# Kernel optimization log

Measured on AMD Instinct MI355X. Metric: run time of the kernel, lower is better.

The kernel has to match this reference:

```python
import jax, jax.numpy as jnp
import numpy as np

B, L, D, H, HD, K, MAXLEN = 4, 2048, 1024, 16, 64, 32, 2048


def setup_inputs() -> dict:
    key = jax.random.key(0)
    ks = jax.random.split(key, 8)
    s = 0.02  # init scale (stand-in for lecun-normal magnitude)
    return {
        "inputs_q": jax.random.normal(ks[0], (B, L, D), jnp.float32),
        "inputs_kv": jax.random.normal(ks[1], (B, L, D), jnp.float32),
        "Wv": jax.random.normal(ks[2], (D, H, HD), jnp.float32) * s,   # value DenseGeneral kernel
        "bv": jnp.zeros((H, HD), jnp.float32),                          # value bias
        "r1": jax.random.normal(ks[3], (H, MAXLEN, K), jnp.float32) * s,  # param 'random1'
        "r2": jax.random.normal(ks[4], (H, K, MAXLEN), jnp.float32) * s,  # param 'random2'
        "Wo": jax.random.normal(ks[5], (H, HD, D), jnp.float32) * s,   # output DenseGeneral kernel
        "bo": jnp.zeros((D,), jnp.float32),                             # output bias
    }


def reference(inputs_q, inputs_kv, Wv, bv, r1, r2, Wo, bo):
    # SynthesizerAttention with ignore_dot_product=True, mode='factorized_random',
    # no masks, deterministic (no dropout).
    qlen = inputs_q.shape[-2]
    kvlen = inputs_kv.shape[-2]
    # value projection: [B, Lkv, H, HD]; key=value, query=inputs_q (unused for scores)
    v = jnp.einsum('bnd,dhk->bnhk', inputs_kv, Wv) + bv
    # factorized random synthetic scores: [H, Lq, Lkv]
    syn = jnp.einsum('hlk,hkn->hln', r1[:, :qlen, :], r2[:, :, :kvlen])
    # softmax over the key/value axis (norm_dims in synthetic_attention).
    # Scores are batch-independent, so softmax once per head (broadcast over B).
    attn = jax.nn.softmax(syn, axis=-1)
    # weighted sum over values: [B, Lq, H, HD]
    y = jnp.einsum('hln,bnhk->blhk', attn, v)
    # output projection over (H, HD): [B, Lq, D]
    return jnp.einsum('blhk,hkd->bld', y, Wo) + bo
```

## Files before the change

kernel.cpp:

```cpp
#include <hip/hip_runtime.h>
#include <hip/hip_bf16.h>

#define LL 2048

typedef __bf16 bf16x8 __attribute__((ext_vector_type(8)));
typedef __bf16 bf16x4 __attribute__((ext_vector_type(4)));
typedef float f32x4 __attribute__((ext_vector_type(4)));

__device__ inline void gl_lds16(const __bf16* g, __bf16* l) {
    __builtin_amdgcn_global_load_lds((const __attribute__((address_space(1))) void*)g,
                                     (__attribute__((address_space(3))) void*)l, 16, 0, 0);
}

__global__ __launch_bounds__(256) void prep(const float* __restrict__ inputs_kv,
                                            const float* __restrict__ r1,
                                            const float* __restrict__ Wv,
                                            const float* __restrict__ Wo,
                                            const float* __restrict__ r2,
                                            __bf16* __restrict__ A1,
                                            __bf16* __restrict__ r1b,
                                            __bf16* __restrict__ Wvt,
                                            __bf16* __restrict__ Wot,
                                            __bf16* __restrict__ r2t) {
    __shared__ float Ls[32][65];
    int bid = blockIdx.x;
    const int tid = threadIdx.x;
    if (bid < 4608) {
        const float* in = (bid < 4096) ? inputs_kv : r1;
        __bf16* out = (bid < 4096) ? A1 : r1b;
        const int t = ((bid < 4096) ? bid : bid - 4096) * 256 + tid;
        const float4* in4 = (const float4*)in;
        float4 f0 = in4[t * 2], f1 = in4[t * 2 + 1];
        bf16x8 o;
        o[0] = (__bf16)f0.x; o[1] = (__bf16)f0.y; o[2] = (__bf16)f0.z; o[3] = (__bf16)f0.w;
        o[4] = (__bf16)f1.x; o[5] = (__bf16)f1.y; o[6] = (__bf16)f1.z; o[7] = (__bf16)f1.w;
        *(bf16x8*)&out[(size_t)t * 8] = o;
        return;
    }
    bid -= 4608;
    const float* in;
    __bf16* out;
    int R, C, r0, c0;
    if (bid < 512) {
        in = Wv; out = Wvt; R = 1024; C = 1024;
        c0 = (bid & 15) * 64; r0 = (bid >> 4) * 32;
    } else if (bid < 1024) {
        bid -= 512;
        in = Wo; out = Wot; R = 1024; C = 1024;
        c0 = (bid & 15) * 64; r0 = (bid >> 4) * 32;
    } else {
        bid -= 1024;
        const int bz = bid >> 5;
        in = r2 + (size_t)bz * 65536; out = r2t + (size_t)bz * 65536;
        R = 32; C = 2048;
        c0 = (bid & 31) * 64; r0 = 0;
    }
#pragma unroll
    for (int p = 0; p < 2; ++p) {
        int f = tid + 256 * p;
        int row = f >> 4, c4 = (f & 15) << 2;
        float4 v = *(const float4*)&in[(size_t)(r0 + row) * C + c0 + c4];
        Ls[row][c4 + 0] = v.x; Ls[row][c4 + 1] = v.y;
        Ls[row][c4 + 2] = v.z; Ls[row][c4 + 3] = v.w;
    }
    __syncthreads();
    const int orow = tid >> 2, rc = (tid & 3) << 3;
    bf16x8 o;
#pragma unroll
    for (int j = 0; j < 8; ++j) o[j] = (__bf16)Ls[rc + j][orow];
    *(bf16x8*)&out[(size_t)(c0 + orow) * R + r0 + rc] = o;
}

template <int MODE>
__global__ __launch_bounds__(256) void gemm_bt(const __bf16* __restrict__ A,
                                               const __bf16* __restrict__ Bt,
                                               const float* __restrict__ bias,
                                               void* __restrict__ Cout,
                                               int M, int N, int K) {
    __shared__ alignas(16) __bf16 As[2][128 * 32];
    const int tid = threadIdx.x;
    const int lane = tid & 63;
    const int wid = __builtin_amdgcn_readfirstlane(tid >> 6);
    const int f = blockIdx.y * 8 + blockIdx.x;
    const int g = (f & 7) * 64 + (f >> 3);
    const int row0 = (g >> 3) * 128, col0 = (g & 7) * 128;
    const int l15 = lane & 15, quad = lane >> 4;
    const int wr = wid & 1, wc = wid >> 1;
    const int s0 = wid * 2, s1 = s0 + 1;

    const __bf16* ga0 = A + (size_t)(row0 + s0 * 16 + (lane >> 2)) * K + ((lane & 3) << 3);
    const __bf16* ga1 = ga0 + (size_t)16 * K;
    const __bf16* gB = Bt + (size_t)(col0 + wc * 64 + l15) * K + quad * 8;

    f32x4 acc[4][4];
#pragma unroll
    for (int i = 0; i < 4; ++i)
#pragma unroll
        for (int j = 0; j < 4; ++j) acc[i][j] = (f32x4){0.f, 0.f, 0.f, 0.f};

    const int nt = K >> 5;
    gl_lds16(ga0, As[0] + s0 * 512);
    gl_lds16(ga1, As[0] + s1 * 512);
    bf16x8 bcur[4], bnxt[4];
#pragma unroll
    for (int j = 0; j < 4; ++j)
        bcur[j] = *(const bf16x8*)(gB + (size_t)j * 16 * K);

    for (int t = 0; t < nt; ++t) {
        __syncthreads();
        if (t + 1 < nt) {
            const int k0 = (t + 1) << 5;
            const int nb = (t + 1) & 1;
            gl_lds16(ga0 + k0, As[nb] + s0 * 512);
            gl_lds16(ga1 + k0, As[nb] + s1 * 512);
#pragma unroll
            for (int j = 0; j < 4; ++j)
                bnxt[j] = *(const bf16x8*)(gB + (size_t)j * 16 * K + k0);
        }
        const __bf16* as = As[t & 1];
        bf16x8 af[4];
#pragma unroll
        for (int i = 0; i < 4; ++i)
            af[i] = *(const bf16x8*)&as[(wr * 64 + i * 16 + l15) * 32 + quad * 8];
#pragma unroll
        for (int i = 0; i < 4; ++i)
#pragma unroll
            for (int j = 0; j < 4; ++j)
                acc[i][j] = __builtin_amdgcn_mfma_f32_16x16x32_bf16(af[i], bcur[j], acc[i][j], 0, 0, 0);
        if (t + 1 < nt) {
#pragma unroll
            for (int j = 0; j < 4; ++j) bcur[j] = bnxt[j];
        }
    }

#pragma unroll
    for (int i = 0; i < 4; ++i) {
        const int rg = row0 + wr * 64 + i * 16 + quad * 4;
#pragma unroll
        for (int j = 0; j < 4; ++j) {
            const int cg = col0 + wc * 64 + j * 16 + l15;
            const float bb = bias[cg];
            if (MODE == 0) {
                const int b = rg >> 11, n = rg & 2047;
                const int h = cg >> 6, hd = cg & 63;
                const int nc = n >> 6, ks = (n >> 5) & 1, qj = (n >> 3) & 3, j0 = n & 7;
                const int jt = hd >> 4, fl = hd & 15;
                __bf16* V3 = (__bf16*)Cout;
                bf16x4 v;
#pragma unroll
                for (int r = 0; r < 4; ++r) v[r] = (__bf16)(acc[i][j][r] + bb);
                *(bf16x4*)&V3[(size_t)(((h * 32 + nc) * 4 + b) * 4096) +
                              (jt * 2 + ks) * 512 + fl * 32 + qj * 8 + j0] = v;
            } else {
                float* Cf = (float*)Cout;
#pragma unroll
                for (int r = 0; r < 4; ++r)
                    Cf[(size_t)(rg + r) * N + cg] = acc[i][j][r] + bb;
            }
        }
    }
}

__global__ __launch_bounds__(512) void attn_pv_v7(const __bf16* __restrict__ r1b,
                                                  const __bf16* __restrict__ r2t,
                                                  const __bf16* __restrict__ V3,
                                                  __bf16* __restrict__ yb) {
    __shared__ alignas(16) __bf16 Ps[2 * 2 * 4 * 1024];
    const int tid = threadIdx.x;
    const int lane = tid & 63;
    const int w = __builtin_amdgcn_readfirstlane(tid >> 6);
    const int b = w & 3, lh = w >> 2;
    const int l15 = lane & 15, quad = lane >> 4;
    const int id = blockIdx.x;
    const int h = id & 15;
    const int l0 = (id >> 4) << 7;

    bf16x8 bf1[4];
#pragma unroll
    for (int i = 0; i < 4; ++i)
        bf1[i] = *(const bf16x8*)&r1b[(size_t)(h * 2048 + l0 + lh * 64 + i * 16 + l15) * 32 + quad * 8];

    const __bf16* r2p = r2t + (size_t)(h * 2048 + b * 16 + l15) * 32 + quad * 8;
    const __bf16* vp = V3 + (size_t)((h * 32) * 4 + b) * 4096 + l15 * 32 + quad * 8;

    bf16x8 r2f = *(const bf16x8*)r2p;
    bf16x8 vpf[4][2];
#pragma unroll
    for (int jt = 0; jt < 4; ++jt)
#pragma unroll
        for (int ks = 0; ks < 2; ++ks)
            vpf[jt][ks] = *(const bf16x8*)(vp + (jt * 2 + ks) * 512);

    bf16x8 ones;
#pragma unroll
    for (int e = 0; e < 8; ++e) ones[e] = (__bf16)1.0f;

    f32x4 acc[4][4];
    f32x4 den[4];
#pragma unroll
    for (int i = 0; i < 4; ++i) {
        den[i] = (f32x4){0.f, 0.f, 0.f, 0.f};
#pragma unroll
        for (int j = 0; j < 4; ++j) acc[i][j] = (f32x4){0.f, 0.f, 0.f, 0.f};
    }
    const f32x4 zero4 = {0.f, 0.f, 0.f, 0.f};

    const int kw = b >> 1;
    const int jg = (b & 1) * 2 + (quad >> 1);
    const int q4 = (quad & 1) * 4;
    const int swz = (l15 >> 1) & 3;

    f32x4 s[4];
#pragma unroll
    for (int i = 0; i < 4; ++i)
        s[i] = __builtin_amdgcn_mfma_f32_16x16x32_bf16(r2f, bf1[i], zero4, 0, 0, 0);
    r2f = *(const bf16x8*)(r2p + 2048);
    {
        __bf16* ps = &Ps[lh * 4096];
#pragma unroll
        for (int i = 0; i < 4; ++i) {
            bf16x4 p4;
#pragma unroll
            for (int r = 0; r < 4; ++r) p4[r] = (__bf16)__expf(s[i][r]);
            *(bf16x4*)&ps[i * 1024 + kw * 512 + l15 * 32 + ((jg ^ swz) << 3) + q4] = p4;
        }
    }

    for (int c = 0; c < 32; ++c) {
        asm volatile("s_waitcnt lgkmcnt(0)" ::: "memory");
        __builtin_amdgcn_s_barrier();
        const __bf16* ps_r = &Ps[((c & 1) * 2 + lh) * 4096];
        bf16x8 pa[4][2];
#pragma unroll
        for (int i = 0; i < 4; ++i)
#pragma unroll
            for (int ks = 0; ks < 2; ++ks)
                pa[i][ks] = *(const bf16x8*)&ps_r[i * 1024 + ks * 512 + l15 * 32 + ((quad ^ swz) << 3)];
#pragma unroll
        for (int i = 0; i < 4; ++i)
            s[i] = __builtin_amdgcn_mfma_f32_16x16x32_bf16(r2f, bf1[i], zero4, 0, 0, 0);
        const int i2 = (c < 30) ? (c + 2) : 31;
        r2f = *(const bf16x8*)(r2p + (size_t)i2 * 2048);
#pragma unroll
        for (int ks = 0; ks < 2; ++ks) {
#pragma unroll
            for (int i = 0; i < 4; ++i) {
#pragma unroll
                for (int jt = 0; jt < 4; ++jt)
                    acc[i][jt] = __builtin_amdgcn_mfma_f32_16x16x32_bf16(pa[i][ks], vpf[jt][ks],
                                                                         acc[i][jt], 0, 0, 0);
                den[i] = __builtin_amdgcn_mfma_f32_16x16x32_bf16(pa[i][ks], ones, den[i], 0, 0, 0);
            }
        }
        __bf16* ps_w = &Ps[(((c + 1) & 1) * 2 + lh) * 4096];
#pragma unroll
        for (int i = 0; i < 4; ++i) {
            bf16x4 p4;
#pragma unroll
            for (int r = 0; r < 4; ++r) p4[r] = (__bf16)__expf(s[i][r]);
            *(bf16x4*)&ps_w[i * 1024 + kw * 512 + l15 * 32 + ((jg ^ swz) << 3) + q4] = p4;
        }
        const int cv = (c < 31) ? 1 : 0;
        vp += cv * 16384;
#pragma unroll
        for (int jt = 0; jt < 4; ++jt)
#pragma unroll
            for (int ks = 0; ks < 2; ++ks)
                vpf[jt][ks] = *(const bf16x8*)(vp + (jt * 2 + ks) * 512);
    }

#pragma unroll
    for (int i = 0; i < 4; ++i) {
#pragma unroll
        for (int r = 0; r < 4; ++r) {
            const float iv = 1.0f / den[i][r];
            const int l = l0 + lh * 64 + i * 16 + quad * 4 + r;
            const size_t rowbase = ((size_t)b * LL + l) * 1024 + h * 64;
#pragma unroll
            for (int jt = 0; jt < 4; ++jt)
                yb[rowbase + jt * 16 + l15] = (__bf16)(acc[i][jt][r] * iv);
        }
    }
}

extern "C" void kernel_launch(void* const* d_in, const int* in_sizes, int n_in,
                              void* d_out, int out_size, void* d_ws, size_t ws_size,
                              hipStream_t stream) {
    const float* inputs_kv = (const float*)d_in[1];
    const float* Wv = (const float*)d_in[2];
    const float* bv = (const float*)d_in[3];
    const float* r1 = (const float*)d_in[4];
    const float* r2 = (const float*)d_in[5];
    const float* Wo = (const float*)d_in[6];
    const float* bo = (const float*)d_in[7];
    float* out = (float*)d_out;

    char* ws = (char*)d_ws;
    const size_t MB = 1024 * 1024;
    __bf16* A1  = (__bf16*)(ws);
    __bf16* Wvt = (__bf16*)(ws + 16 * MB);
    __bf16* Wot = (__bf16*)(ws + 18 * MB);
    __bf16* r1b = (__bf16*)(ws + 20 * MB);
    __bf16* r2t = (__bf16*)(ws + 22 * MB);
    __bf16* V3  = (__bf16*)(ws + 24 * MB);
    __bf16* yb  = (__bf16*)(ws + 40 * MB);

    prep<<<6144, 256, 0, stream>>>(inputs_kv, r1, Wv, Wo, r2, A1, r1b, Wvt, Wot, r2t);
    gemm_bt<0><<<dim3(8, 64), 256, 0, stream>>>(A1, Wvt, bv, V3, 8192, 1024, 1024);
    attn_pv_v7<<<256, 512, 0, stream>>>(r1b, r2t, V3, yb);
    gemm_bt<1><<<dim3(8, 64), 256, 0, stream>>>(yb, Wot, bo, out, 8192, 1024, 1024);
}
```

Before: 233.8 us.

## Stage B tiles through LDS with triple-buffered async loads in gemm_bt

The B operand in the projection GEMMs is now loaded into LDS through direct global-to-LDS copies instead of per-wave register loads, and both A and B use a three-stage ring buffer with prefetch distance two. Explicit vmcnt waits plus a raw barrier replace the single syncthreads, so loads for future tiles stay in flight during the MFMAs. This is meant to hide global load latency and remove the duplicated B fetches across waves. In exchange it uses more LDS, which can lower occupancy, and it relies on hand-counted vmcnt values being correct.

```diff
diff --git a/kernel.cpp b/kernel.cpp
--- a/kernel.cpp
+++ b/kernel.cpp
@@ -77,7 +77,8 @@
                                                const float* __restrict__ bias,
                                                void* __restrict__ Cout,
                                                int M, int N, int K) {
-    __shared__ alignas(16) __bf16 As[2][128 * 32];
+    __shared__ alignas(16) __bf16 As[3][128 * 32];
+    __shared__ alignas(16) __bf16 Bs[3][128 * 32];
     const int tid = threadIdx.x;
     const int lane = tid & 63;
     const int wid = __builtin_amdgcn_readfirstlane(tid >> 6);
@@ -90,7 +91,8 @@
 
     const __bf16* ga0 = A + (size_t)(row0 + s0 * 16 + (lane >> 2)) * K + ((lane & 3) << 3);
     const __bf16* ga1 = ga0 + (size_t)16 * K;
-    const __bf16* gB = Bt + (size_t)(col0 + wc * 64 + l15) * K + quad * 8;
+    const __bf16* gb0 = Bt + (size_t)(col0 + s0 * 16 + (lane >> 2)) * K + ((lane & 3) << 3);
+    const __bf16* gb1 = gb0 + (size_t)16 * K;
 
     f32x4 acc[4][4];
 #pragma unroll
@@ -99,38 +101,49 @@
         for (int j = 0; j < 4; ++j) acc[i][j] = (f32x4){0.f, 0.f, 0.f, 0.f};
 
     const int nt = K >> 5;
+
     gl_lds16(ga0, As[0] + s0 * 512);
     gl_lds16(ga1, As[0] + s1 * 512);
-    bf16x8 bcur[4], bnxt[4];
-#pragma unroll
-    for (int j = 0; j < 4; ++j)
-        bcur[j] = *(const bf16x8*)(gB + (size_t)j * 16 * K);
-
+    gl_lds16(gb0, Bs[0] + s0 * 512);
+    gl_lds16(gb1, Bs[0] + s1 * 512);
+    if (nt > 1) {
+        gl_lds16(ga0 + 32, As[1] + s0 * 512);
+        gl_lds16(ga1 + 32, As[1] + s1 * 512);
+        gl_lds16(gb0 + 32, Bs[1] + s0 * 512);
+        gl_lds16(gb1 + 32, Bs[1] + s1 * 512);
+    }
+
+    int cur = 0;
     for (int t = 0; t < nt; ++t) {
-        __syncthreads();
         if (t + 1 < nt) {
-            const int k0 = (t + 1) << 5;
-            const int nb = (t + 1) & 1;
+            asm volatile("s_waitcnt vmcnt(4)" ::: "memory");
+        } else {
+            asm volatile("s_waitcnt vmcnt(0)" ::: "memory");
+        }
+        __builtin_amdgcn_s_barrier();
+        if (t + 2 < nt) {
+            int nb = cur + 2; if (nb >= 3) nb -= 3;
+            const int k0 = (t + 2) << 5;
             gl_lds16(ga0 + k0, As[nb] + s0 * 512);
             gl_lds16(ga1 + k0, As[nb] + s1 * 512);
-#pragma unroll
-            for (int j = 0; j < 4; ++j)
-                bnxt[j] = *(const bf16x8*)(gB + (size_t)j * 16 * K + k0);
-        }
-        const __bf16* as = As[t & 1];
-        bf16x8 af[4];
+            gl_lds16(gb0 + k0, Bs[nb] + s0 * 512);
+            gl_lds16(gb1 + k0, Bs[nb] + s1 * 512);
+        }
+        const __bf16* as = As[cur];
+        const __bf16* bs = Bs[cur];
+        bf16x8 af[4], bfv[4];
 #pragma unroll
         for (int i = 0; i < 4; ++i)
             af[i] = *(const bf16x8*)&as[(wr * 64 + i * 16 + l15) * 32 + quad * 8];
 #pragma unroll
+        for (int j = 0; j < 4; ++j)
+            bfv[j] = *(const bf16x8*)&bs[(wc * 64 + j * 16 + l15) * 32 + quad * 8];
+#pragma unroll
         for (int i = 0; i < 4; ++i)
 #pragma unroll
             for (int j = 0; j < 4; ++j)
-                acc[i][j] = __builtin_amdgcn_mfma_f32_16x16x32_bf16(af[i], bcur[j], acc[i][j], 0, 0, 0);
-        if (t + 1 < nt) {
-#pragma unroll
-            for (int j = 0; j < 4; ++j) bcur[j] = bnxt[j];
-        }
+                acc[i][j] = __builtin_amdgcn_mfma_f32_16x16x32_bf16(af[i], bfv[j], acc[i][j], 0, 0, 0);
+        cur = (cur + 1 == 3) ? 0 : cur + 1;
     }
 
 #pragma unroll
```

New measurement: 211.2 us. 9.7% less time.

## Stage both GEMM operands through swizzled LDS with BK=64 double buffering

Applied to the files above, without the earlier changes.

The gemm_bt kernel now stages both A and B tiles into LDS with direct global-to-LDS loads, using a K-step of 64 instead of 32. An XOR swizzle on 16-byte chunks is meant to avoid LDS bank conflicts. Previously B fragments were loaded straight from global memory into registers, with each wave fetching them separately. The aim is to halve the number of barriers per K and to get B reuse and coalescing through LDS. The cost is four times the LDS footprint (64KB total), which may lower occupancy.

```diff
diff --git a/kernel.cpp b/kernel.cpp
--- a/kernel.cpp
+++ b/kernel.cpp
@@ -77,7 +77,8 @@
                                                const float* __restrict__ bias,
                                                void* __restrict__ Cout,
                                                int M, int N, int K) {
-    __shared__ alignas(16) __bf16 As[2][128 * 32];
+    __shared__ alignas(16) __bf16 As[2][128 * 64];
+    __shared__ alignas(16) __bf16 Bs[2][128 * 64];
     const int tid = threadIdx.x;
     const int lane = tid & 63;
     const int wid = __builtin_amdgcn_readfirstlane(tid >> 6);
@@ -86,11 +87,12 @@
     const int row0 = (g >> 3) * 128, col0 = (g & 7) * 128;
     const int l15 = lane & 15, quad = lane >> 4;
     const int wr = wid & 1, wc = wid >> 1;
-    const int s0 = wid * 2, s1 = s0 + 1;
-
-    const __bf16* ga0 = A + (size_t)(row0 + s0 * 16 + (lane >> 2)) * K + ((lane & 3) << 3);
-    const __bf16* ga1 = ga0 + (size_t)16 * K;
-    const __bf16* gB = Bt + (size_t)(col0 + wc * 64 + l15) * K + quad * 8;
+
+    const int srow = wid * 32 + (lane >> 3);
+    const int skoff = (((lane & 7) ^ (lane >> 3)) << 3);
+    const __bf16* gaS = A + (size_t)(row0 + srow) * K + skoff;
+    const __bf16* gbS = Bt + (size_t)(col0 + srow) * K + skoff;
+    const int lbase = (wid * 32) * 64;
 
     f32x4 acc[4][4];
 #pragma unroll
@@ -98,40 +100,50 @@
 #pragma unroll
         for (int j = 0; j < 4; ++j) acc[i][j] = (f32x4){0.f, 0.f, 0.f, 0.f};
 
-    const int nt = K >> 5;
-    gl_lds16(ga0, As[0] + s0 * 512);
-    gl_lds16(ga1, As[0] + s1 * 512);
-    bf16x8 bcur[4], bnxt[4];
-#pragma unroll
-    for (int j = 0; j < 4; ++j)
-        bcur[j] = *(const bf16x8*)(gB + (size_t)j * 16 * K);
+    const int nt = K >> 6;
+
+#define STAGE(buf, k0)                                                        \
+    {                                                                         \
+        _Pragma("unroll")                                                     \
+        for (int q = 0; q < 4; ++q) {                                         \
+            gl_lds16(gaS + (size_t)(q * 8) * K + (k0), As[buf] + lbase + q * 512); \
+            gl_lds16(gbS + (size_t)(q * 8) * K + (k0), Bs[buf] + lbase + q * 512); \
+        }                                                                     \
+    }
+
+    STAGE(0, 0)
 
     for (int t = 0; t < nt; ++t) {
         __syncthreads();
         if (t + 1 < nt) {
-            const int k0 = (t + 1) << 5;
-            const int nb = (t + 1) & 1;
-            gl_lds16(ga0 + k0, As[nb] + s0 * 512);
-            gl_lds16(ga1 + k0, As[nb] + s1 * 512);
-#pragma unroll
-            for (int j = 0; j < 4; ++j)
-                bnxt[j] = *(const bf16x8*)(gB + (size_t)j * 16 * K + k0);
+            const int k0 = (t + 1) << 6;
+            if ((t & 1) == 0) STAGE(1, k0) else STAGE(0, k0)
         }
         const __bf16* as = As[t & 1];
-        bf16x8 af[4];
-#pragma unroll
-        for (int i = 0; i < 4; ++i)
-            af[i] = *(const bf16x8*)&as[(wr * 64 + i * 16 + l15) * 32 + quad * 8];
-#pragma unroll
-        for (int i = 0; i < 4; ++i)
-#pragma unroll
-            for (int j = 0; j < 4; ++j)
-                acc[i][j] = __builtin_amdgcn_mfma_f32_16x16x32_bf16(af[i], bcur[j], acc[i][j], 0, 0, 0);
-        if (t + 1 < nt) {
-#pragma unroll
-            for (int j = 0; j < 4; ++j) bcur[j] = bnxt[j];
-        }
-    }
+        const __bf16* bs = Bs[t & 1];
+#pragma unroll
+        for (int ksub = 0; ksub < 2; ++ksub) {
+            bf16x8 af[4], bfv[4];
+#pragma unroll
+            for (int i = 0; i < 4; ++i) {
+                const int r = wr * 64 + i * 16 + l15;
+                const int ch = (ksub * 4 + quad) ^ (l15 & 7);
+                af[i] = *(const bf16x8*)&as[r * 64 + ch * 8];
+            }
+#pragma unroll
+            for (int j = 0; j < 4; ++j) {
+                const int r = wc * 64 + j * 16 + l15;
+                const int ch = (ksub * 4 + quad) ^ (l15 & 7);
+                bfv[j] = *(const bf16x8*)&bs[r * 64 + ch * 8];
+            }
+#pragma unroll
+            for (int i = 0; i < 4; ++i)
+#pragma unroll
+                for (int j = 0; j < 4; ++j)
+                    acc[i][j] = __builtin_amdgcn_mfma_f32_16x16x32_bf16(af[i], bfv[j], acc[i][j], 0, 0, 0);
+        }
+    }
+#undef STAGE
 
 #pragma unroll
     for (int i = 0; i < 4; ++i) {
```

Result: faster. 201.3 us (-13.9%).
